# Performance work log

Measured on AMD Instinct MI355X. Metric: run time of the kernel, lower is better.

The kernel has to match this reference:

```python
import jax, jax.numpy as jnp
import numpy as np

QUANT = 6                      # quant bits
LEVELS = 2 ** QUANT - 1        # quant_levels = 63


def setup_inputs() -> dict:
    key = jax.random.key(0)
    k1, k2, k3 = jax.random.split(key, 3)
    B, C_in, C_out, H, W = 8, 256, 256, 64, 64
    x = jax.random.normal(k1, (B, C_in, H, W), dtype=jnp.float32)
    # 1x1 conv weight stored as [out_channels, in_channels] (kernel dims are 1)
    weight = jax.random.normal(k2, (C_out, C_in), dtype=jnp.float32) * 0.05
    bias = jax.random.normal(k3, (C_out,), dtype=jnp.float32) * 0.05
    return {"x": x, "weight": weight, "bias": bias}


def reference(x, weight, bias):
    """NoiseConv.forward with hard_weight set, mode='batch':
    channel_wise_quantize -> hardware_inference -> float cast.
    (Original computes in float64 on CUDA; here float32 for jit/accel friendliness.)
    """
    # --- channel_wise_quantize (input is detached in torch) ---
    xd = jax.lax.stop_gradient(x)
    cmax = jnp.max(xd, axis=1, keepdims=True)           # [B,1,H,W]
    cmin = jnp.min(xd, axis=1, keepdims=True)           # [B,1,H,W]
    scaling = (cmax - cmin) / LEVELS                    # [B,1,H,W]
    x_int = jnp.round((xd - cmin) / scaling).astype(jnp.int32)  # [B,C,H,W] in [0,63]
    bit_idx = jnp.arange(QUANT, dtype=jnp.int32)
    bits = ((x_int[..., None] >> bit_idx) & 1).astype(x.dtype)   # [B,C,H,W,Q] bitplanes

    # --- hardware_inference (batch mode): one 1x1 conv per bitplane, then
    # weighted recombination with 2^b. Fused here into a single einsum; the
    # math is identical since conv is linear and bitplane values are exact. ---
    base = (2.0 ** jnp.arange(QUANT)).astype(x.dtype)   # quant_base
    out_sum = jnp.einsum('bchwq,q,oc->bohw', bits, base, weight)  # [B,O,H,W]
    out_w = out_sum * scaling                           # per-pixel rescale

    # min-offset term: conv2d(cmin * ones_like(x_plane), weight, bias).
    # cmin is constant across input channels, so it equals cmin * sum_c(w) + bias.
    wsum = jnp.sum(weight, axis=1)                      # [O]
    out_w = out_w + cmin * wsum[None, :, None, None] + bias[None, :, None, None]

    return out_w.astype(jnp.float32)
```

## Files before the change

kernel.cpp:

```cpp
#include <hip/hip_runtime.h>
#include <stdint.h>

#define CI 256
#define CO 256
#define HW 4096
#define PT 64

typedef __attribute__((ext_vector_type(8))) short short8;
typedef __attribute__((ext_vector_type(4))) float float4v;

__global__ void prep_kernel(const float* __restrict__ w,
                            ushort* __restrict__ w16,
                            float* __restrict__ wsum) {
    const int o = blockIdx.x;
    const int lane = threadIdx.x;
    float4 v = ((const float4*)(w + o * CI))[lane];
    auto cvt = [](float f) -> ushort {
        uint32_t u = __float_as_uint(f);
        return (ushort)((u + 0x7FFFu + ((u >> 16) & 1u)) >> 16);
    };
    ushort4 q;
    q.x = cvt(v.x); q.y = cvt(v.y); q.z = cvt(v.z); q.w = cvt(v.w);
    ((ushort4*)(w16 + o * CI))[lane] = q;
    float s = v.x + v.y + v.z + v.w;
    for (int off = 32; off >= 1; off >>= 1) s += __shfl_down(s, off);
    if (lane == 0) wsum[o] = s;
}

__global__ __launch_bounds__(256)
void noise_conv_kernel(const float* __restrict__ x,
                       const ushort* __restrict__ w16,
                       const float* __restrict__ wsum,
                       const float* __restrict__ bias,
                       float* __restrict__ out) {
    const int t = threadIdx.x;
    const int lane = t & 63;
    const int wv = t >> 6;
    const int n16 = lane & 15;
    const int quad = lane >> 4;

    const int blk = blockIdx.x;
    const int img = blk >> 6;
    const int p0 = (blk & 63) * PT;
    const int pix = p0 + wv * 16 + n16;
    const float* xb = x + (size_t)img * CI * HW;

    float xv[64];
    #pragma unroll
    for (int tt = 0; tt < 8; ++tt)
        #pragma unroll
        for (int j = 0; j < 8; ++j)
            xv[tt * 8 + j] = xb[(size_t)(quad * 8 + 32 * tt + j) * HW + pix];

    float mn = xv[0], mx = xv[0];
    #pragma unroll
    for (int i = 1; i < 64; ++i) { mn = fminf(mn, xv[i]); mx = fmaxf(mx, xv[i]); }
    mn = fminf(mn, __shfl_xor(mn, 16));
    mx = fmaxf(mx, __shfl_xor(mx, 16));
    mn = fminf(mn, __shfl_xor(mn, 32));
    mx = fmaxf(mx, __shfl_xor(mx, 32));

    const float cm = mn;
    const float sc = (mx - mn) / 63.0f;
    const float iv = 1.0f / sc;

    short8 afr[8];
    #pragma unroll
    for (int tt = 0; tt < 8; ++tt) {
        union { short8 s; uint32_t u[4]; } fr;
        #pragma unroll
        for (int j2 = 0; j2 < 4; ++j2) {
            const float q0 = rintf((xv[tt * 8 + 2 * j2]     - cm) * iv);
            const float q1 = rintf((xv[tt * 8 + 2 * j2 + 1] - cm) * iv);
            fr.u[j2] = (__float_as_uint(q0) >> 16) |
                       (__float_as_uint(q1) & 0xFFFF0000u);
        }
        afr[tt] = fr.s;
    }

    float4v acc[16];
    #pragma unroll
    for (int nt = 0; nt < 16; ++nt) {
        float4v z = {0.0f, 0.0f, 0.0f, 0.0f};
        acc[nt] = z;
    }
    #pragma unroll
    for (int tt = 0; tt < 8; ++tt) {
        const short8 af = afr[tt];
        #pragma unroll
        for (int nt = 0; nt < 16; ++nt) {
            const short8 bf = *((const short8*)(
                w16 + (size_t)(nt * 16 + n16) * CI + tt * 32 + quad * 8));
            acc[nt] = __builtin_amdgcn_mfma_f32_16x16x32_bf16(af, bf, acc[nt], 0, 0, 0);
        }
    }

    float sv[4], cv[4];
    #pragma unroll
    for (int r = 0; r < 4; ++r) {
        sv[r] = __shfl(sc, quad * 4 + r);
        cv[r] = __shfl(cm, quad * 4 + r);
    }
    float* outb = out + (size_t)img * CO * HW + p0 + wv * 16 + quad * 4;
    #pragma unroll
    for (int nt = 0; nt < 16; ++nt) {
        const int ch = nt * 16 + n16;
        const float ws = wsum[ch];
        const float bs = bias[ch];
        float4 o;
        o.x = acc[nt][0] * sv[0] + cv[0] * ws + bs;
        o.y = acc[nt][1] * sv[1] + cv[1] * ws + bs;
        o.z = acc[nt][2] * sv[2] + cv[2] * ws + bs;
        o.w = acc[nt][3] * sv[3] + cv[3] * ws + bs;
        *((float4*)(outb + (size_t)ch * HW)) = o;
    }
}

extern "C" void kernel_launch(void* const* d_in, const int* in_sizes, int n_in,
                              void* d_out, int out_size, void* d_ws, size_t ws_size,
                              hipStream_t stream) {
    const float* x    = (const float*)d_in[0];
    const float* w    = (const float*)d_in[1];
    const float* bias = (const float*)d_in[2];
    float* out = (float*)d_out;

    ushort* w16 = (ushort*)d_ws;
    float* wsum = (float*)((char*)d_ws + (size_t)CO * CI * sizeof(ushort));

    prep_kernel<<<CO, 64, 0, stream>>>(w, w16, wsum);
    noise_conv_kernel<<<512, 256, 0, stream>>>(x, w16, wsum, bias, out);
}
```

Measured before the change: 118.5 us.

## Stage quantized activations in LDS and split output channels across waves

The block tile shrinks to 32 pixels and the grid doubles. All 256 threads now load input channels for the min/max reduction, combining partial results through shared memory. The quantized bf16 activations go into a padded LDS tile, and each wave computes 64 output channels across all 32 pixels instead of all 256 channels for 16 pixels. This should cut per-wave weight loads and register pressure (16 accumulators down to 8, xv array halved) and raise occupancy. The cost is extra LDS traffic and three block barriers.

```diff
diff --git a/kernel.cpp b/kernel.cpp
--- a/kernel.cpp
+++ b/kernel.cpp
@@ -4,7 +4,8 @@
 #define CI 256
 #define CO 256
 #define HW 4096
-#define PT 64
+#define PXT 32
+#define QP 264
 
 typedef __attribute__((ext_vector_type(8))) short short8;
 typedef __attribute__((ext_vector_type(4))) float float4v;
@@ -33,86 +34,118 @@
                        const float* __restrict__ wsum,
                        const float* __restrict__ bias,
                        float* __restrict__ out) {
+    __shared__ ushort Q[PXT * QP];
+    __shared__ float Rmn[8][33], Rmx[8][33];
+    __shared__ float cmin_s[PXT], s_s[PXT], inv_s[PXT];
+
     const int t = threadIdx.x;
-    const int lane = t & 63;
-    const int wv = t >> 6;
-    const int n16 = lane & 15;
-    const int quad = lane >> 4;
+    const int blk = blockIdx.x;
+    const int img = blk >> 7;
+    const int p0 = (blk & 127) * PXT;
+    const float* xb = x + (size_t)img * CI * HW + p0;
 
-    const int blk = blockIdx.x;
-    const int img = blk >> 6;
-    const int p0 = (blk & 63) * PT;
-    const int pix = p0 + wv * 16 + n16;
-    const float* xb = x + (size_t)img * CI * HW;
+    const int p = t & 31;
+    const int cg = t >> 5;
 
-    float xv[64];
+    float xv[32];
     #pragma unroll
-    for (int tt = 0; tt < 8; ++tt)
-        #pragma unroll
-        for (int j = 0; j < 8; ++j)
-            xv[tt * 8 + j] = xb[(size_t)(quad * 8 + 32 * tt + j) * HW + pix];
+    for (int j = 0; j < 32; ++j)
+        xv[j] = xb[(size_t)(cg * 32 + j) * HW + p];
 
     float mn = xv[0], mx = xv[0];
     #pragma unroll
-    for (int i = 1; i < 64; ++i) { mn = fminf(mn, xv[i]); mx = fmaxf(mx, xv[i]); }
-    mn = fminf(mn, __shfl_xor(mn, 16));
-    mx = fmaxf(mx, __shfl_xor(mx, 16));
-    mn = fminf(mn, __shfl_xor(mn, 32));
-    mx = fmaxf(mx, __shfl_xor(mx, 32));
+    for (int j = 1; j < 32; ++j) { mn = fminf(mn, xv[j]); mx = fmaxf(mx, xv[j]); }
+    Rmn[cg][p] = mn;
+    Rmx[cg][p] = mx;
+    __syncthreads();
+    if (t < 32) {
+        float m0 = Rmn[0][t], m1 = Rmx[0][t];
+        #pragma unroll
+        for (int s = 1; s < 8; ++s) {
+            m0 = fminf(m0, Rmn[s][t]);
+            m1 = fmaxf(m1, Rmx[s][t]);
+        }
+        const float sc = (m1 - m0) / 63.0f;
+        cmin_s[t] = m0;
+        s_s[t] = sc;
+        inv_s[t] = 1.0f / sc;
+    }
+    __syncthreads();
 
-    const float cm = mn;
-    const float sc = (mx - mn) / 63.0f;
-    const float iv = 1.0f / sc;
+    {
+        const float cm = cmin_s[p];
+        const float iv = inv_s[p];
+        uint32_t pk[16];
+        #pragma unroll
+        for (int j2 = 0; j2 < 16; ++j2) {
+            const float q0 = rintf((xv[2 * j2]     - cm) * iv);
+            const float q1 = rintf((xv[2 * j2 + 1] - cm) * iv);
+            pk[j2] = (__float_as_uint(q0) >> 16) |
+                     (__float_as_uint(q1) & 0xFFFF0000u);
+        }
+        ushort* qrow = Q + p * QP + cg * 32;
+        #pragma unroll
+        for (int v = 0; v < 4; ++v)
+            ((uint4*)qrow)[v] = make_uint4(pk[4 * v], pk[4 * v + 1],
+                                           pk[4 * v + 2], pk[4 * v + 3]);
+    }
+    __syncthreads();
 
-    short8 afr[8];
+    const int l = t & 63;
+    const int wv = t >> 6;
+    const int m16 = l & 15;
+    const int quad = l >> 4;
+
+    float4v acc[2][4];
     #pragma unroll
-    for (int tt = 0; tt < 8; ++tt) {
-        union { short8 s; uint32_t u[4]; } fr;
+    for (int mt = 0; mt < 2; ++mt)
         #pragma unroll
-        for (int j2 = 0; j2 < 4; ++j2) {
-            const float q0 = rintf((xv[tt * 8 + 2 * j2]     - cm) * iv);
-            const float q1 = rintf((xv[tt * 8 + 2 * j2 + 1] - cm) * iv);
-            fr.u[j2] = (__float_as_uint(q0) >> 16) |
-                       (__float_as_uint(q1) & 0xFFFF0000u);
+        for (int nt = 0; nt < 4; ++nt) {
+            float4v z = {0.0f, 0.0f, 0.0f, 0.0f};
+            acc[mt][nt] = z;
         }
-        afr[tt] = fr.s;
-    }
 
-    float4v acc[16];
+    const ushort* wrow = w16 + (size_t)(wv * 64) * CI;
     #pragma unroll
-    for (int nt = 0; nt < 16; ++nt) {
-        float4v z = {0.0f, 0.0f, 0.0f, 0.0f};
-        acc[nt] = z;
-    }
-    #pragma unroll
-    for (int tt = 0; tt < 8; ++tt) {
-        const short8 af = afr[tt];
+    for (int ks = 0; ks < 8; ++ks) {
+        short8 af[2];
         #pragma unroll
-        for (int nt = 0; nt < 16; ++nt) {
+        for (int mt = 0; mt < 2; ++mt)
+            af[mt] = *((const short8*)(
+                Q + (mt * 16 + m16) * QP + ks * 32 + quad * 8));
+        #pragma unroll
+        for (int nt = 0; nt < 4; ++nt) {
             const short8 bf = *((const short8*)(
-                w16 + (size_t)(nt * 16 + n16) * CI + tt * 32 + quad * 8));
-            acc[nt] = __builtin_amdgcn_mfma_f32_16x16x32_bf16(af, bf, acc[nt], 0, 0, 0);
+                wrow + (size_t)(nt * 16 + m16) * CI + ks * 32 + quad * 8));
+            #pragma unroll
+            for (int mt = 0; mt < 2; ++mt)
+                acc[mt][nt] = __builtin_amdgcn_mfma_f32_16x16x32_bf16(
+                    af[mt], bf, acc[mt][nt], 0, 0, 0);
         }
     }
 
-    float sv[4], cv[4];
+    float* outp = out + (size_t)img * CO * HW + p0;
     #pragma unroll
-    for (int r = 0; r < 4; ++r) {
-        sv[r] = __shfl(sc, quad * 4 + r);
-        cv[r] = __shfl(cm, quad * 4 + r);
-    }
-    float* outb = out + (size_t)img * CO * HW + p0 + wv * 16 + quad * 4;
-    #pragma unroll
-    for (int nt = 0; nt < 16; ++nt) {
-        const int ch = nt * 16 + n16;
-        const float ws = wsum[ch];
-        const float bs = bias[ch];
-        float4 o;
-        o.x = acc[nt][0] * sv[0] + cv[0] * ws + bs;
-        o.y = acc[nt][1] * sv[1] + cv[1] * ws + bs;
-        o.z = acc[nt][2] * sv[2] + cv[2] * ws + bs;
-        o.w = acc[nt][3] * sv[3] + cv[3] * ws + bs;
-        *((float4*)(outb + (size_t)ch * HW)) = o;
+    for (int mt = 0; mt < 2; ++mt) {
+        const int pb = mt * 16 + quad * 4;
+        float sv[4], cv[4];
+        #pragma unroll
+        for (int r = 0; r < 4; ++r) {
+            sv[r] = s_s[pb + r];
+            cv[r] = cmin_s[pb + r];
+        }
+        #pragma unroll
+        for (int nt = 0; nt < 4; ++nt) {
+            const int ch = wv * 64 + nt * 16 + m16;
+            const float ws = wsum[ch];
+            const float bs = bias[ch];
+            float4 o;
+            o.x = acc[mt][nt][0] * sv[0] + cv[0] * ws + bs;
+            o.y = acc[mt][nt][1] * sv[1] + cv[1] * ws + bs;
+            o.z = acc[mt][nt][2] * sv[2] + cv[2] * ws + bs;
+            o.w = acc[mt][nt][3] * sv[3] + cv[3] * ws + bs;
+            *((float4*)(outp + (size_t)ch * HW + pb)) = o;
+        }
     }
 }
 
@@ -128,5 +161,5 @@
     float* wsum = (float*)((char*)d_ws + (size_t)CO * CI * sizeof(ushort));
 
     prep_kernel<<<CO, 64, 0, stream>>>(w, w16, wsum);
-    noise_conv_kernel<<<512, 256, 0, stream>>>(x, w16, wsum, bias, out);
+    noise_conv_kernel<<<1024, 256, 0, stream>>>(x, w16, wsum, bias, out);
 }
```

Measured after the change: 101.4 us. 1.17x faster.
